# Kernel tuning notes

Measured on AMD Instinct MI355X. Metric: run time of the kernel, lower is better.

## Reference

```python
import jax, jax.numpy as jnp
import numpy as np

EPS = 1e-5  # BatchNorm eps (torch default)

def setup_inputs() -> dict:
    key = jax.random.key(0)
    ks = jax.random.split(key, 12)
    B, C, H, W = 4, 256, 64, 64
    IC = 128  # inter_channels = C // 2
    s = 1.0 / np.sqrt(C)
    si = 1.0 / np.sqrt(IC)
    return {
        "x": jax.random.normal(ks[0], (B, C, H, W), jnp.float32),
        "y": jax.random.normal(ks[1], (B, C, H, W), jnp.float32),
        "g_w": jax.random.normal(ks[2], (IC, C), jnp.float32) * s,
        "g_b": jax.random.normal(ks[3], (IC,), jnp.float32) * 0.01,
        "dx_w": jax.random.normal(ks[4], (IC, C), jnp.float32) * s,
        "dx_b": jax.random.normal(ks[5], (IC,), jnp.float32) * 0.01,
        "dy_w": jax.random.normal(ks[6], (IC, C), jnp.float32) * s,
        "dy_b": jax.random.normal(ks[7], (IC,), jnp.float32) * 0.01,
        "w_w": jax.random.normal(ks[8], (C, IC), jnp.float32) * si,
        "w_b": jax.random.normal(ks[9], (C,), jnp.float32) * 0.01,
        "bn_gamma": jax.random.normal(ks[10], (C,), jnp.float32),
        "bn_beta": jax.random.normal(ks[11], (C,), jnp.float32) * 0.01,
    }

def _conv1x1(t, w, b):
    # t: [B,C,H,W], w: [O,C], b: [O] -> [B,O,H,W]
    return jnp.einsum('bchw,oc->bohw', t, w) + b[None, :, None, None]

def reference(x, y, g_w, g_b, dx_w, dx_b, dy_w, dy_b, w_w, w_b, bn_gamma, bn_beta):
    B, C, H, W = x.shape
    IC = g_w.shape[0]
    N = H * W
    g_y = _conv1x1(y, g_w, g_b).reshape(B, IC, N).transpose(0, 2, 1)      # [B,N,IC]
    theta_x = _conv1x1(x, dx_w, dx_b).reshape(B, IC, N).transpose(0, 2, 1)  # [B,N,IC]
    phi_y = _conv1x1(y, dy_w, dy_b).reshape(B, IC, N)                      # [B,IC,N]
    f = jnp.einsum('bnc,bcm->bnm', theta_x, phi_y)                         # [B,N,N]
    f_div_C = jax.nn.softmax(f, axis=-1)
    y2 = jnp.einsum('bnm,bmc->bnc', f_div_C, g_y)                          # [B,N,IC]
    y2 = y2.transpose(0, 2, 1).reshape(B, IC, H, W)
    wy = _conv1x1(y2, w_w, w_b)                                            # [B,C,H,W]
    # BatchNorm2d in training mode: batch stats over (B,H,W) per channel
    mean = jnp.mean(wy, axis=(0, 2, 3), keepdims=True)
    var = jnp.var(wy, axis=(0, 2, 3), keepdims=True)
    wy_bn = (wy - mean) / jnp.sqrt(var + EPS)
    wy_bn = wy_bn * bn_gamma[None, :, None, None] + bn_beta[None, :, None, None]
    return wy_bn + x
```

## Files before the change

### kernel.cpp

```cpp
#include <hip/hip_runtime.h>
#include <hip/hip_bf16.h>
#include <math.h>

typedef unsigned short ushort_t;
typedef __attribute__((ext_vector_type(8))) short   short8;
typedef __attribute__((ext_vector_type(8))) unsigned short ushort8;
typedef __attribute__((ext_vector_type(4))) float   float4v;

__device__ __forceinline__ float b2f(ushort_t u) {
    return __uint_as_float(((unsigned)u) << 16);
}
__device__ __forceinline__ ushort_t f2b(float f) {
    unsigned i = __float_as_uint(f);
    return (ushort_t)((i + 0x7FFFu + ((i >> 16) & 1u)) >> 16);
}
__device__ __forceinline__ void split2(float v, ushort_t& h, ushort_t& l) {
    h = f2b(v);
    l = f2b(v - b2f(h));
}
__device__ __forceinline__ void glds16(const ushort_t* g, ushort_t* l) {
    __builtin_amdgcn_global_load_lds((const __attribute__((address_space(1))) void*)g,
                                     (__attribute__((address_space(3))) void*)l, 16, 0, 0);
}

#define WTFH_OFF   0
#define WTFL_OFF   196608
#define WWBH_OFF   393216
#define WWBL_OFF   458752
#define BIAS_OFF   524288
#define STATS_OFF  526336
#define PROJH_OFF  1048576
#define PROJL_OFF  9437184
#define GT_OFF     17825792
#define OPART_OFF  22020096
#define WY_OFF     1048576

__global__ void prep_k(const float* __restrict__ dx_w, const float* __restrict__ dy_w,
                       const float* __restrict__ g_w,  const float* __restrict__ dx_b,
                       const float* __restrict__ dy_b, const float* __restrict__ g_b,
                       const float* __restrict__ w_w,
                       ushort_t* __restrict__ wtfh, ushort_t* __restrict__ wtfl,
                       ushort_t* __restrict__ wwbh, ushort_t* __restrict__ wwbl,
                       float* __restrict__ bias) {
    int idx = blockIdx.x * 256 + threadIdx.x;
    int j = idx & 7, lane = (idx >> 3) & 63, kk = (idx >> 9) & 7, ot = idx >> 12;
    int o = ot * 16 + (lane & 15);
    int c = kk * 32 + ((lane >> 4) * 8) + j;
    float v;
    if (o < 128)      v = dx_w[o * 256 + c];
    else if (o < 256) v = dy_w[(o - 128) * 256 + c];
    else              v = g_w[(o - 256) * 256 + c];
    ushort_t h, l;
    split2(v, h, l);
    wtfh[idx] = h; wtfl[idx] = l;
    if (idx < 32768) {
        split2(w_w[idx], h, l);
        wwbh[idx] = h; wwbl[idx] = l;
    }
    if (idx < 384) {
        bias[idx] = (idx < 128) ? dx_b[idx]
                  : (idx < 256) ? dy_b[idx - 128]
                                : g_b[idx - 256];
    }
}

__global__ __launch_bounds__(256) void proj_k(const float* __restrict__ x,
                                              const float* __restrict__ y,
                                              const ushort_t* __restrict__ wtfh,
                                              const ushort_t* __restrict__ wtfl,
                                              const float* __restrict__ bias,
                                              ushort_t* __restrict__ projh,
                                              ushort_t* __restrict__ projl,
                                              ushort_t* __restrict__ gT) {
    __shared__ ushort_t xT[2][32 * 256];
    int b = blockIdx.y, n0 = blockIdx.x * 32;
    int tid = threadIdx.x;
    int w = tid >> 6, lane = tid & 63;
    int mrow = lane & 15, quad = lane >> 4, koff = quad * 8;
    int half = w & 1, sect = w >> 1;
    int arow = half * 16 + mrow;

    for (int s = 0; s < 2; s++) {
        if (s) __syncthreads();
        const float* src = s ? y : x;
        #pragma unroll
        for (int i = 0; i < 4; i++) {
            int ch = tid + i * 256;
            int c = ch >> 2, off = (ch & 3) * 8;
            const float* p = src + (size_t)(b * 256 + c) * 4096 + n0 + off;
            float4v v0 = *(const float4v*)p;
            float4v v1 = *(const float4v*)(p + 4);
            #pragma unroll
            for (int jj = 0; jj < 4; jj++) {
                ushort_t h, l;
                split2(v0[jj], h, l);
                xT[0][(off + jj) * 256 + c] = h;
                xT[1][(off + jj) * 256 + c] = l;
                split2(v1[jj], h, l);
                xT[0][(off + 4 + jj) * 256 + c] = h;
                xT[1][(off + 4 + jj) * 256 + c] = l;
            }
        }
        __syncthreads();

        short8 fh[8], fl[8];
        #pragma unroll
        for (int kk = 0; kk < 8; kk++) {
            fh[kk] = *(const short8*)&xT[0][arow * 256 + kk * 32 + koff];
            fl[kk] = *(const short8*)&xT[1][arow * 256 + kk * 32 + koff];
        }

        int ot0 = s ? (8 + sect * 8) : (sect * 4);
        int ot1 = s ? (ot0 + 8) : (ot0 + 4);
        for (int ot = ot0; ot < ot1; ot++) {
            float4v acc = {0.f, 0.f, 0.f, 0.f};
            #pragma unroll
            for (int kk = 0; kk < 8; kk++) {
                short8 bh = *(const short8*)(wtfh + (size_t)((ot * 8 + kk) * 64 + lane) * 8);
                short8 bl = *(const short8*)(wtfl + (size_t)((ot * 8 + kk) * 64 + lane) * 8);
                acc = __builtin_amdgcn_mfma_f32_16x16x32_bf16(fh[kk], bh, acc, 0, 0, 0);
                acc = __builtin_amdgcn_mfma_f32_16x16x32_bf16(fh[kk], bl, acc, 0, 0, 0);
                acc = __builtin_amdgcn_mfma_f32_16x16x32_bf16(fl[kk], bh, acc, 0, 0, 0);
            }
            int o = ot * 16 + mrow;
            float bo = bias[o];
            #pragma unroll
            for (int r = 0; r < 4; r++) {
                int n = n0 + half * 16 + quad * 4 + r;
                float v = acc[r] + bo;
                if (ot < 16) {
                    ushort_t h, l;
                    split2(v, h, l);
                    projh[(size_t)(b * 4096 + n) * 256 + o] = h;
                    projl[(size_t)(b * 4096 + n) * 256 + o] = l;
                } else {
                    gT[(size_t)(b * 128 + (o - 256)) * 4096 + n] = f2b(v);
                }
            }
        }
    }
}

__global__ __launch_bounds__(256, 2) void flash_k(const ushort_t* __restrict__ projh,
                                                  const ushort_t* __restrict__ projl,
                                                  const ushort_t* __restrict__ gT,
                                                  float* __restrict__ opart,
                                                  float* __restrict__ oml,
                                                  int kqlog) {
    __shared__ __align__(16) ushort_t KshF[8192];
    __shared__ __align__(16) ushort_t KslF[8192];
    __shared__ __align__(16) ushort_t VsF[8192];
    ushort_t* Ps = KshF;

    int b = blockIdx.y;
    int kq = blockIdx.x & ((1 << kqlog) - 1);
    int q0 = (blockIdx.x >> kqlog) * 128;
    int iters = 64 >> kqlog;
    int kt0 = kq * iters;
    int tid = threadIdx.x, w = tid >> 6, lane = tid & 63;
    int mrow = lane & 15, quad = lane >> 4, koff = quad * 8;

    int kRow[4], kCol[4], vIc[4], vOf[4];
    #pragma unroll
    for (int i = 0; i < 4; i++) {
        int ck = tid + i * 256, combo = ck >> 6, l2 = ck & 63;
        kRow[i] = (combo >> 2) * 16 + (l2 & 15);
        kCol[i] = 128 + (combo & 3) * 32 + (l2 >> 4) * 8;
        vIc[i]  = (combo >> 1) * 16 + (l2 & 15);
        vOf[i]  = (combo & 1) * 32 + (l2 >> 4) * 8;
    }

    short8 qfh[2][4], qfl[2][4];
    #pragma unroll
    for (int s = 0; s < 2; s++)
        #pragma unroll
        for (int kk = 0; kk < 4; kk++) {
            size_t qoff = (size_t)(b * 4096 + q0 + w * 32 + s * 16 + mrow) * 256 + kk * 32 + koff;
            qfh[s][kk] = *(const short8*)(projh + qoff);
            qfl[s][kk] = *(const short8*)(projl + qoff);
        }

    float l_i[2][4];
    float4v oacc[2][8];
    #pragma unroll
    for (int s = 0; s < 2; s++) {
        #pragma unroll
        for (int r = 0; r < 4; r++) l_i[s][r] = 0.f;
        #pragma unroll
        for (int ot = 0; ot < 8; ot++) oacc[s][ot] = (float4v){0.f, 0.f, 0.f, 0.f};
    }

    for (int kt = kt0; kt < kt0 + iters; kt++) {
        int kb = kt * 64;
        __syncthreads();
        #pragma unroll
        for (int i = 0; i < 4; i++) {
            int dst = (i * 256 + w * 64) * 8;
            glds16(projh + (size_t)(b * 4096 + kb + kRow[i]) * 256 + kCol[i], &KshF[dst]);
            glds16(projl + (size_t)(b * 4096 + kb + kRow[i]) * 256 + kCol[i], &KslF[dst]);
            glds16(gT + (size_t)(b * 128 + vIc[i]) * 4096 + kb + vOf[i], &VsF[dst]);
        }
        __syncthreads();

        float4v sacc[2][4];
        #pragma unroll
        for (int ct = 0; ct < 4; ct++) {
            float4v a0 = {0.f, 0.f, 0.f, 0.f}, a1 = {0.f, 0.f, 0.f, 0.f};
            #pragma unroll
            for (int kk = 0; kk < 4; kk++) {
                short8 bh = *(const short8*)&KshF[((ct * 4 + kk) * 64 + lane) * 8];
                short8 bl = *(const short8*)&KslF[((ct * 4 + kk) * 64 + lane) * 8];
                a0 = __builtin_amdgcn_mfma_f32_16x16x32_bf16(qfh[0][kk], bh, a0, 0, 0, 0);
                a1 = __builtin_amdgcn_mfma_f32_16x16x32_bf16(qfh[1][kk], bh, a1, 0, 0, 0);
                a0 = __builtin_amdgcn_mfma_f32_16x16x32_bf16(qfh[0][kk], bl, a0, 0, 0, 0);
                a1 = __builtin_amdgcn_mfma_f32_16x16x32_bf16(qfh[1][kk], bl, a1, 0, 0, 0);
                a0 = __builtin_amdgcn_mfma_f32_16x16x32_bf16(qfl[0][kk], bh, a0, 0, 0, 0);
                a1 = __builtin_amdgcn_mfma_f32_16x16x32_bf16(qfl[1][kk], bh, a1, 0, 0, 0);
            }
            sacc[0][ct] = a0; sacc[1][ct] = a1;
        }
        __syncthreads();

        #pragma unroll
        for (int s = 0; s < 2; s++)
            #pragma unroll
            for (int r = 0; r < 4; r++) {
                float p0 = __builtin_exp2f(fmaf(sacc[s][0][r], 1.44269504f, -92.332481f));
                float p1 = __builtin_exp2f(fmaf(sacc[s][1][r], 1.44269504f, -92.332481f));
                float p2 = __builtin_exp2f(fmaf(sacc[s][2][r], 1.44269504f, -92.332481f));
                float p3 = __builtin_exp2f(fmaf(sacc[s][3][r], 1.44269504f, -92.332481f));
                float rs = (p0 + p1) + (p2 + p3);
                #pragma unroll
                for (int d = 1; d < 16; d <<= 1) rs += __shfl_xor(rs, d, 64);
                l_i[s][r] += rs;
                int prow = w * 32 + s * 16 + quad * 4 + r;
                Ps[prow * 72 +  0 + mrow] = f2b(p0);
                Ps[prow * 72 + 16 + mrow] = f2b(p1);
                Ps[prow * 72 + 32 + mrow] = f2b(p2);
                Ps[prow * 72 + 48 + mrow] = f2b(p3);
            }
        __builtin_amdgcn_s_waitcnt(0xC07F);

        #pragma unroll
        for (int k2 = 0; k2 < 2; k2++) {
            short8 a0 = *(const short8*)&Ps[(w * 32 + mrow) * 72 + k2 * 32 + koff];
            short8 a1 = *(const short8*)&Ps[(w * 32 + 16 + mrow) * 72 + k2 * 32 + koff];
            #pragma unroll
            for (int ot = 0; ot < 8; ot++) {
                short8 bfr = *(const short8*)&VsF[((ot * 2 + k2) * 64 + lane) * 8];
                oacc[0][ot] = __builtin_amdgcn_mfma_f32_16x16x32_bf16(a0, bfr, oacc[0][ot], 0, 0, 0);
                oacc[1][ot] = __builtin_amdgcn_mfma_f32_16x16x32_bf16(a1, bfr, oacc[1][ot], 0, 0, 0);
            }
        }
    }

    #pragma unroll
    for (int s = 0; s < 2; s++)
        #pragma unroll
        for (int ot = 0; ot < 8; ot++)
            #pragma unroll
            for (int r = 0; r < 4; r++) {
                int R = b * 4096 + q0 + w * 32 + s * 16 + quad * 4 + r;
                opart[((size_t)kq * 16384 + R) * 128 + ot * 16 + mrow] = oacc[s][ot][r];
            }
    if (mrow == 0) {
        #pragma unroll
        for (int s = 0; s < 2; s++)
            #pragma unroll
            for (int r = 0; r < 4; r++) {
                int R = b * 4096 + q0 + w * 32 + s * 16 + quad * 4 + r;
                oml[kq * 16384 + R] = l_i[s][r];
            }
    }
}

__global__ __launch_bounds__(256) void wy_k(const float* __restrict__ opart,
                                            const float* __restrict__ oml,
                                            const ushort_t* __restrict__ wwbh,
                                            const ushort_t* __restrict__ wwbl,
                                            const float* __restrict__ w_b,
                                            ushort_t* __restrict__ wy, int KQ) {
    int b = blockIdx.y, n0 = blockIdx.x * 32;
    int tid = threadIdx.x, w = tid >> 6, lane = tid & 63;
    int mrow = lane & 15, quad = lane >> 4, koff = quad * 8;
    int half = w & 1, sect = w >> 1;
    int Rn = b * 4096 + n0 + half * 16 + mrow;

    float L = 0.f;
    for (int kq = 0; kq < KQ; kq++) L += oml[kq * 16384 + Rn];
    float invL = 1.f / L;

    short8 bfh[4], bfl[4];
    #pragma unroll
    for (int kk = 0; kk < 4; kk++) {
        float a[8];
        #pragma unroll
        for (int j = 0; j < 8; j++) a[j] = 0.f;
        for (int kq = 0; kq < KQ; kq++) {
            const float* p = opart + ((size_t)kq * 16384 + Rn) * 128 + kk * 32 + koff;
            float4v v0 = *(const float4v*)p;
            float4v v1 = *(const float4v*)(p + 4);
            #pragma unroll
            for (int j = 0; j < 4; j++) { a[j] += v0[j]; a[4 + j] += v1[j]; }
        }
        #pragma unroll
        for (int j = 0; j < 8; j++) {
            ushort_t h, l;
            split2(a[j] * invL, h, l);
            bfh[kk][j] = (short)h; bfl[kk][j] = (short)l;
        }
    }

    int coln = n0 + half * 16 + mrow;
    for (int cot = sect * 8; cot < sect * 8 + 8; cot++) {
        float4v acc = {0.f, 0.f, 0.f, 0.f};
        #pragma unroll
        for (int kk = 0; kk < 4; kk++) {
            size_t woff = (size_t)(cot * 16 + mrow) * 128 + kk * 32 + koff;
            short8 ah = *(const short8*)(wwbh + woff);
            short8 al = *(const short8*)(wwbl + woff);
            acc = __builtin_amdgcn_mfma_f32_16x16x32_bf16(ah, bfh[kk], acc, 0, 0, 0);
            acc = __builtin_amdgcn_mfma_f32_16x16x32_bf16(ah, bfl[kk], acc, 0, 0, 0);
            acc = __builtin_amdgcn_mfma_f32_16x16x32_bf16(al, bfh[kk], acc, 0, 0, 0);
        }
        #pragma unroll
        for (int r = 0; r < 4; r++) {
            int co = cot * 16 + quad * 4 + r;
            wy[(size_t)(b * 256 + co) * 4096 + coln] = f2b(acc[r] + w_b[co]);
        }
    }
}

__global__ __launch_bounds__(256) void stats_k(const ushort_t* __restrict__ wy,
                                               float* __restrict__ stats) {
    __shared__ float red[8];
    int co = blockIdx.x, tid = threadIdx.x, w = tid >> 6, lane = tid & 63;
    float s = 0.f, s2 = 0.f;
    #pragma unroll
    for (int i = 0; i < 8; i++) {
        int ch = tid + i * 256;
        int b = ch >> 9, n = (ch & 511) * 8;
        ushort8 v = *(const ushort8*)(wy + (size_t)(b * 256 + co) * 4096 + n);
        #pragma unroll
        for (int j = 0; j < 8; j++) { float f = b2f(v[j]); s += f; s2 += f * f; }
    }
    #pragma unroll
    for (int d = 1; d < 64; d <<= 1) { s += __shfl_xor(s, d, 64); s2 += __shfl_xor(s2, d, 64); }
    if (lane == 0) { red[w] = s; red[4 + w] = s2; }
    __syncthreads();
    if (tid == 0) {
        stats[co]       = red[0] + red[1] + red[2] + red[3];
        stats[256 + co] = red[4] + red[5] + red[6] + red[7];
    }
}

__global__ __launch_bounds__(256) void bn_k(const ushort_t* __restrict__ wy,
                                            const float* __restrict__ x,
                                            const float* __restrict__ gamma,
                                            const float* __restrict__ beta,
                                            const float* __restrict__ stats,
                                            float* __restrict__ out) {
    int idx = (blockIdx.x * 256 + threadIdx.x) * 8;
    int c = (idx >> 12) & 255;
    const float inv_cnt = 1.f / 16384.f;
    float mean = stats[c] * inv_cnt;
    float var  = stats[256 + c] * inv_cnt - mean * mean;
    float inv  = rsqrtf(var + 1e-5f);
    float scale = gamma[c] * inv;
    float shift = beta[c] - mean * scale;
    ushort8 wv = *(const ushort8*)(wy + idx);
    float4v x0 = *(const float4v*)(x + idx);
    float4v x1 = *(const float4v*)(x + idx + 4);
    float4v o0, o1;
    #pragma unroll
    for (int j = 0; j < 4; j++) {
        o0[j] = b2f(wv[j]) * scale + shift + x0[j];
        o1[j] = b2f(wv[4 + j]) * scale + shift + x1[j];
    }
    *(float4v*)(out + idx) = o0;
    *(float4v*)(out + idx + 4) = o1;
}

extern "C" void kernel_launch(void* const* d_in, const int* in_sizes, int n_in,
                              void* d_out, int out_size, void* d_ws, size_t ws_size,
                              hipStream_t stream) {
    const float* x    = (const float*)d_in[0];
    const float* y    = (const float*)d_in[1];
    const float* g_w  = (const float*)d_in[2];
    const float* g_b  = (const float*)d_in[3];
    const float* dx_w = (const float*)d_in[4];
    const float* dx_b = (const float*)d_in[5];
    const float* dy_w = (const float*)d_in[6];
    const float* dy_b = (const float*)d_in[7];
    const float* w_w  = (const float*)d_in[8];
    const float* w_b  = (const float*)d_in[9];
    const float* bn_g = (const float*)d_in[10];
    const float* bn_b = (const float*)d_in[11];

    char* ws = (char*)d_ws;
    ushort_t* wtfh  = (ushort_t*)(ws + WTFH_OFF);
    ushort_t* wtfl  = (ushort_t*)(ws + WTFL_OFF);
    ushort_t* wwbh  = (ushort_t*)(ws + WWBH_OFF);
    ushort_t* wwbl  = (ushort_t*)(ws + WWBL_OFF);
    float*    bias  = (float*)(ws + BIAS_OFF);
    float*    stats = (float*)(ws + STATS_OFF);
    ushort_t* projh = (ushort_t*)(ws + PROJH_OFF);
    ushort_t* projl = (ushort_t*)(ws + PROJL_OFF);
    ushort_t* gT    = (ushort_t*)(ws + GT_OFF);
    float*    opart = (float*)(ws + OPART_OFF);
    ushort_t* wy    = (ushort_t*)(ws + WY_OFF);
    float*    out   = (float*)d_out;

    int kqlog;
    if      (ws_size >= 22020096u + 4u * 8388608u + 4u * 65536u) kqlog = 2;
    else if (ws_size >= 22020096u + 2u * 8388608u + 2u * 65536u) kqlog = 1;
    else                                                         kqlog = 0;
    int KQ = 1 << kqlog;
    float* oml = (float*)(ws + OPART_OFF + (size_t)KQ * 8388608u);

    prep_k<<<384, 256, 0, stream>>>(dx_w, dy_w, g_w, dx_b, dy_b, g_b, w_w,
                                    wtfh, wtfl, wwbh, wwbl, bias);
    proj_k<<<dim3(128, 4), 256, 0, stream>>>(x, y, wtfh, wtfl, bias, projh, projl, gT);
    flash_k<<<dim3(32 << kqlog, 4), 256, 0, stream>>>(projh, projl, gT, opart, oml, kqlog);
    wy_k<<<dim3(128, 4), 256, 0, stream>>>(opart, oml, wwbh, wwbl, w_b, wy, KQ);
    stats_k<<<256, 256, 0, stream>>>(wy, stats);
    bn_k<<<2048, 256, 0, stream>>>(wy, x, bn_g, bn_b, stats, out);
}
```

Baseline: 254.7 us.

## Use fp16 Q/K with single MFMA, double-buffer K/V tiles, MFMA row sums

Stores the theta/phi projections as a single fp16 copy instead of a bf16 hi/lo split, which cuts the QK^T MFMA count threefold and halves K traffic. The flash kernel now uses 512 threads and 256 query rows per block, double-buffers the K and V tiles in LDS so the next tile loads while the current one computes, and drops a barrier. Softmax row sums move from shuffle reductions to an extra MFMA against a vector of ones. The costs are lower score precision (fp16 with a fixed exponent offset, so there is overflow/accuracy risk), more LDS per block, and fewer blocks in flight.

```diff
diff --git a/kernel.cpp b/kernel.cpp
--- a/kernel.cpp
+++ b/kernel.cpp
@@ -3,9 +3,10 @@
 #include <math.h>
 
 typedef unsigned short ushort_t;
-typedef __attribute__((ext_vector_type(8))) short   short8;
+typedef __attribute__((ext_vector_type(8))) short     short8;
+typedef __attribute__((ext_vector_type(8))) _Float16  half8;
 typedef __attribute__((ext_vector_type(8))) unsigned short ushort8;
-typedef __attribute__((ext_vector_type(4))) float   float4v;
+typedef __attribute__((ext_vector_type(4))) float     float4v;
 
 __device__ __forceinline__ float b2f(ushort_t u) {
     return __uint_as_float(((unsigned)u) << 16);
@@ -29,10 +30,9 @@
 #define WWBL_OFF   458752
 #define BIAS_OFF   524288
 #define STATS_OFF  526336
-#define PROJH_OFF  1048576
-#define PROJL_OFF  9437184
-#define GT_OFF     17825792
-#define OPART_OFF  22020096
+#define PROJF_OFF  1048576
+#define GT_OFF     9437184
+#define OPART_OFF  13631488
 #define WY_OFF     1048576
 
 __global__ void prep_k(const float* __restrict__ dx_w, const float* __restrict__ dy_w,
@@ -69,8 +69,7 @@
                                               const ushort_t* __restrict__ wtfh,
                                               const ushort_t* __restrict__ wtfl,
                                               const float* __restrict__ bias,
-                                              ushort_t* __restrict__ projh,
-                                              ushort_t* __restrict__ projl,
+                                              ushort_t* __restrict__ projf,
                                               ushort_t* __restrict__ gT) {
     __shared__ ushort_t xT[2][32 * 256];
     int b = blockIdx.y, n0 = blockIdx.x * 32;
@@ -129,10 +128,8 @@
                 int n = n0 + half * 16 + quad * 4 + r;
                 float v = acc[r] + bo;
                 if (ot < 16) {
-                    ushort_t h, l;
-                    split2(v, h, l);
-                    projh[(size_t)(b * 4096 + n) * 256 + o] = h;
-                    projl[(size_t)(b * 4096 + n) * 256 + o] = l;
+                    _Float16 hf = (_Float16)v;
+                    projf[(size_t)(b * 4096 + n) * 256 + o] = *(ushort_t*)&hf;
                 } else {
                     gT[(size_t)(b * 128 + (o - 256)) * 4096 + n] = f2b(v);
                 }
@@ -141,66 +138,73 @@
     }
 }
 
-__global__ __launch_bounds__(256, 2) void flash_k(const ushort_t* __restrict__ projh,
-                                                  const ushort_t* __restrict__ projl,
+__global__ __launch_bounds__(512, 2) void flash_k(const ushort_t* __restrict__ projf,
                                                   const ushort_t* __restrict__ gT,
                                                   float* __restrict__ opart,
                                                   float* __restrict__ oml,
                                                   int kqlog) {
-    __shared__ __align__(16) ushort_t KshF[8192];
-    __shared__ __align__(16) ushort_t KslF[8192];
-    __shared__ __align__(16) ushort_t VsF[8192];
-    ushort_t* Ps = KshF;
+    __shared__ __align__(16) ushort_t KsF[2][8192];
+    __shared__ __align__(16) ushort_t VsF[2][8192];
+    __shared__ __align__(16) ushort_t Ps[256 * 72];
 
     int b = blockIdx.y;
     int kq = blockIdx.x & ((1 << kqlog) - 1);
-    int q0 = (blockIdx.x >> kqlog) * 128;
+    int q0 = (blockIdx.x >> kqlog) * 256;
     int iters = 64 >> kqlog;
     int kt0 = kq * iters;
     int tid = threadIdx.x, w = tid >> 6, lane = tid & 63;
     int mrow = lane & 15, quad = lane >> 4, koff = quad * 8;
 
-    int kRow[4], kCol[4], vIc[4], vOf[4];
-    #pragma unroll
-    for (int i = 0; i < 4; i++) {
-        int ck = tid + i * 256, combo = ck >> 6, l2 = ck & 63;
+    int kRow[2], kCol[2], vIc[2], vOf[2], dstB[2];
+    #pragma unroll
+    for (int i = 0; i < 2; i++) {
+        int ck = tid + i * 512, combo = ck >> 6, l2 = ck & 63;
         kRow[i] = (combo >> 2) * 16 + (l2 & 15);
         kCol[i] = 128 + (combo & 3) * 32 + (l2 >> 4) * 8;
         vIc[i]  = (combo >> 1) * 16 + (l2 & 15);
         vOf[i]  = (combo & 1) * 32 + (l2 >> 4) * 8;
-    }
-
-    short8 qfh[2][4], qfl[2][4];
+        dstB[i] = (i * 512 + w * 64) * 8;
+    }
+
+    half8 qf[2][4];
     #pragma unroll
     for (int s = 0; s < 2; s++)
         #pragma unroll
-        for (int kk = 0; kk < 4; kk++) {
-            size_t qoff = (size_t)(b * 4096 + q0 + w * 32 + s * 16 + mrow) * 256 + kk * 32 + koff;
-            qfh[s][kk] = *(const short8*)(projh + qoff);
-            qfl[s][kk] = *(const short8*)(projl + qoff);
-        }
-
-    float l_i[2][4];
-    float4v oacc[2][8];
+        for (int kk = 0; kk < 4; kk++)
+            qf[s][kk] = *(const half8*)(projf + (size_t)(b * 4096 + q0 + w * 32 + s * 16 + mrow) * 256
+                                        + kk * 32 + koff);
+
+    float4v oacc[2][8], oaccL[2];
     #pragma unroll
     for (int s = 0; s < 2; s++) {
-        #pragma unroll
-        for (int r = 0; r < 4; r++) l_i[s][r] = 0.f;
+        oaccL[s] = (float4v){0.f, 0.f, 0.f, 0.f};
         #pragma unroll
         for (int ot = 0; ot < 8; ot++) oacc[s][ot] = (float4v){0.f, 0.f, 0.f, 0.f};
     }
+    short8 vones;
+    #pragma unroll
+    for (int j = 0; j < 8; j++) vones[j] = (short)0x3F80;
+
+    {
+        int kb = kt0 * 64;
+        #pragma unroll
+        for (int i = 0; i < 2; i++) {
+            glds16(projf + (size_t)(b * 4096 + kb + kRow[i]) * 256 + kCol[i], &KsF[0][dstB[i]]);
+            glds16(gT + (size_t)(b * 128 + vIc[i]) * 4096 + kb + vOf[i], &VsF[0][dstB[i]]);
+        }
+    }
 
     for (int kt = kt0; kt < kt0 + iters; kt++) {
-        int kb = kt * 64;
+        int cur = (kt - kt0) & 1;
         __syncthreads();
-        #pragma unroll
-        for (int i = 0; i < 4; i++) {
-            int dst = (i * 256 + w * 64) * 8;
-            glds16(projh + (size_t)(b * 4096 + kb + kRow[i]) * 256 + kCol[i], &KshF[dst]);
-            glds16(projl + (size_t)(b * 4096 + kb + kRow[i]) * 256 + kCol[i], &KslF[dst]);
-            glds16(gT + (size_t)(b * 128 + vIc[i]) * 4096 + kb + vOf[i], &VsF[dst]);
-        }
-        __syncthreads();
+        if (kt + 1 < kt0 + iters) {
+            int kb = (kt + 1) * 64;
+            #pragma unroll
+            for (int i = 0; i < 2; i++) {
+                glds16(projf + (size_t)(b * 4096 + kb + kRow[i]) * 256 + kCol[i], &KsF[1 - cur][dstB[i]]);
+                glds16(gT + (size_t)(b * 128 + vIc[i]) * 4096 + kb + vOf[i], &VsF[1 - cur][dstB[i]]);
+            }
+        }
 
         float4v sacc[2][4];
         #pragma unroll
@@ -208,36 +212,23 @@
             float4v a0 = {0.f, 0.f, 0.f, 0.f}, a1 = {0.f, 0.f, 0.f, 0.f};
             #pragma unroll
             for (int kk = 0; kk < 4; kk++) {
-                short8 bh = *(const short8*)&KshF[((ct * 4 + kk) * 64 + lane) * 8];
-                short8 bl = *(const short8*)&KslF[((ct * 4 + kk) * 64 + lane) * 8];
-                a0 = __builtin_amdgcn_mfma_f32_16x16x32_bf16(qfh[0][kk], bh, a0, 0, 0, 0);
-                a1 = __builtin_amdgcn_mfma_f32_16x16x32_bf16(qfh[1][kk], bh, a1, 0, 0, 0);
-                a0 = __builtin_amdgcn_mfma_f32_16x16x32_bf16(qfh[0][kk], bl, a0, 0, 0, 0);
-                a1 = __builtin_amdgcn_mfma_f32_16x16x32_bf16(qfh[1][kk], bl, a1, 0, 0, 0);
-                a0 = __builtin_amdgcn_mfma_f32_16x16x32_bf16(qfl[0][kk], bh, a0, 0, 0, 0);
-                a1 = __builtin_amdgcn_mfma_f32_16x16x32_bf16(qfl[1][kk], bh, a1, 0, 0, 0);
+                half8 bh = *(const half8*)&KsF[cur][((ct * 4 + kk) * 64 + lane) * 8];
+                a0 = __builtin_amdgcn_mfma_f32_16x16x32_f16(qf[0][kk], bh, a0, 0, 0, 0);
+                a1 = __builtin_amdgcn_mfma_f32_16x16x32_f16(qf[1][kk], bh, a1, 0, 0, 0);
             }
             sacc[0][ct] = a0; sacc[1][ct] = a1;
         }
-        __syncthreads();
 
         #pragma unroll
         for (int s = 0; s < 2; s++)
             #pragma unroll
             for (int r = 0; r < 4; r++) {
-                float p0 = __builtin_exp2f(fmaf(sacc[s][0][r], 1.44269504f, -92.332481f));
-                float p1 = __builtin_exp2f(fmaf(sacc[s][1][r], 1.44269504f, -92.332481f));
-                float p2 = __builtin_exp2f(fmaf(sacc[s][2][r], 1.44269504f, -92.332481f));
-                float p3 = __builtin_exp2f(fmaf(sacc[s][3][r], 1.44269504f, -92.332481f));
-                float rs = (p0 + p1) + (p2 + p3);
+                int prow = w * 32 + s * 16 + quad * 4 + r;
                 #pragma unroll
-                for (int d = 1; d < 16; d <<= 1) rs += __shfl_xor(rs, d, 64);
-                l_i[s][r] += rs;
-                int prow = w * 32 + s * 16 + quad * 4 + r;
-                Ps[prow * 72 +  0 + mrow] = f2b(p0);
-                Ps[prow * 72 + 16 + mrow] = f2b(p1);
-                Ps[prow * 72 + 32 + mrow] = f2b(p2);
-                Ps[prow * 72 + 48 + mrow] = f2b(p3);
+                for (int ct = 0; ct < 4; ct++) {
+                    float p = __builtin_exp2f(fmaf(sacc[s][ct][r], 1.44269504f, -92.332481f));
+                    Ps[prow * 72 + ct * 16 + mrow] = f2b(p);
+                }
             }
         __builtin_amdgcn_s_waitcnt(0xC07F);
 
@@ -247,10 +238,12 @@
             short8 a1 = *(const short8*)&Ps[(w * 32 + 16 + mrow) * 72 + k2 * 32 + koff];
             #pragma unroll
             for (int ot = 0; ot < 8; ot++) {
-                short8 bfr = *(const short8*)&VsF[((ot * 2 + k2) * 64 + lane) * 8];
+                short8 bfr = *(const short8*)&VsF[cur][((ot * 2 + k2) * 64 + lane) * 8];
                 oacc[0][ot] = __builtin_amdgcn_mfma_f32_16x16x32_bf16(a0, bfr, oacc[0][ot], 0, 0, 0);
                 oacc[1][ot] = __builtin_amdgcn_mfma_f32_16x16x32_bf16(a1, bfr, oacc[1][ot], 0, 0, 0);
             }
+            oaccL[0] = __builtin_amdgcn_mfma_f32_16x16x32_bf16(a0, vones, oaccL[0], 0, 0, 0);
+            oaccL[1] = __builtin_amdgcn_mfma_f32_16x16x32_bf16(a1, vones, oaccL[1], 0, 0, 0);
         }
     }
 
@@ -269,7 +262,7 @@
             #pragma unroll
             for (int r = 0; r < 4; r++) {
                 int R = b * 4096 + q0 + w * 32 + s * 16 + quad * 4 + r;
-                oml[kq * 16384 + R] = l_i[s][r];
+                oml[kq * 16384 + R] = oaccL[s][r];
             }
     }
 }
@@ -404,24 +397,23 @@
     ushort_t* wwbl  = (ushort_t*)(ws + WWBL_OFF);
     float*    bias  = (float*)(ws + BIAS_OFF);
     float*    stats = (float*)(ws + STATS_OFF);
-    ushort_t* projh = (ushort_t*)(ws + PROJH_OFF);
-    ushort_t* projl = (ushort_t*)(ws + PROJL_OFF);
+    ushort_t* projf = (ushort_t*)(ws + PROJF_OFF);
     ushort_t* gT    = (ushort_t*)(ws + GT_OFF);
     float*    opart = (float*)(ws + OPART_OFF);
     ushort_t* wy    = (ushort_t*)(ws + WY_OFF);
     float*    out   = (float*)d_out;
 
     int kqlog;
-    if      (ws_size >= 22020096u + 4u * 8388608u + 4u * 65536u) kqlog = 2;
-    else if (ws_size >= 22020096u + 2u * 8388608u + 2u * 65536u) kqlog = 1;
-    else                                                         kqlog = 0;
+    if      (ws_size >= 13631488u + 4u * (8388608u + 65536u)) kqlog = 2;
+    else if (ws_size >= 13631488u + 2u * (8388608u + 65536u)) kqlog = 1;
+    else                                                      kqlog = 0;
     int KQ = 1 << kqlog;
     float* oml = (float*)(ws + OPART_OFF + (size_t)KQ * 8388608u);
 
     prep_k<<<384, 256, 0, stream>>>(dx_w, dy_w, g_w, dx_b, dy_b, g_b, w_w,
                                     wtfh, wtfl, wwbh, wwbl, bias);
-    proj_k<<<dim3(128, 4), 256, 0, stream>>>(x, y, wtfh, wtfl, bias, projh, projl, gT);
-    flash_k<<<dim3(32 << kqlog, 4), 256, 0, stream>>>(projh, projl, gT, opart, oml, kqlog);
+    proj_k<<<dim3(128, 4), 256, 0, stream>>>(x, y, wtfh, wtfl, bias, projf, gT);
+    flash_k<<<dim3(16 << kqlog, 4), 512, 0, stream>>>(projf, gT, opart, oml, kqlog);
     wy_k<<<dim3(128, 4), 256, 0, stream>>>(opart, oml, wwbh, wwbl, w_b, wy, KQ);
     stats_k<<<256, 256, 0, stream>>>(wy, stats);
     bn_k<<<2048, 256, 0, stream>>>(wy, x, bn_g, bn_b, stats, out);
```

Measured after the change: 222.5 us. -12.6%, faster.
